# Performance work log

Hardware: AMD Instinct MI355X
Metric: run time of the kernel (lower is better)

Reference implementation:

```python
import jax, jax.numpy as jnp
import numpy as np

# PtConv dims from SegSmall: pl=64 channels, n_centers=16 kernel elements, dim=3
B, N, K = 4, 16384, 16          # batch, points, neighbors
C_IN, C_OUT, KS, DIM = 64, 64, 16, 3


def setup_inputs() -> dict:
    key = jax.random.key(0)
    ks = jax.random.split(key, 10)
    features = jax.random.normal(ks[0], (B, N, C_IN), dtype=jnp.float32)
    input_pts = jax.random.uniform(ks[1], (B, N, DIM), dtype=jnp.float32)
    output_pts = input_pts  # same-resolution conv: queries == input points
    indices = jax.random.randint(ks[2], (B, N, K), 0, N)  # precomputed KNN indices
    # weight init as in PtConv
    bound = float(np.sqrt(3.0) * np.sqrt(2.0 / (C_IN + C_OUT)))
    weight = jax.random.uniform(ks[3], (C_IN, KS, C_OUT), jnp.float32, -bound, bound)
    bias = jnp.zeros((C_OUT,), jnp.float32)
    centers = jax.random.uniform(ks[4], (DIM, KS), jnp.float32, -1.0, 1.0)
    # position-MLP params: Linear(dim*KS -> 2*KS), Linear(2*KS -> KS), Linear(KS -> KS)
    def lin(k, fan_in, fan_out):
        lim = 1.0 / np.sqrt(fan_in)
        kw, kb = jax.random.split(k)
        W = jax.random.uniform(kw, (fan_in, fan_out), jnp.float32, -lim, lim)
        b = jax.random.uniform(kb, (fan_out,), jnp.float32, -lim, lim)
        return W, b
    w1, b1 = lin(ks[5], DIM * KS, 2 * KS)
    w2, b2 = lin(ks[6], 2 * KS, KS)
    w3, b3 = lin(ks[7], KS, KS)
    return {"features": features, "input_pts": input_pts, "output_pts": output_pts,
            "weight": weight, "bias": bias, "centers": centers,
            "w1": w1, "b1": b1, "w2": w2, "b2": b2, "w3": w3, "b3": b3,
            "indices": indices}


def reference(features, input_pts, output_pts, weight, bias, centers,
              w1, b1, w2, b2, w3, b3, indices):
    # per-batch gather of neighbor features and coordinates
    gather = jax.vmap(lambda a, idx: a[idx])
    feat_g = gather(features, indices)          # [B, M, K, C_in]
    pts_g = gather(input_pts, indices)          # [B, M, K, 3]
    pts = pts_g - output_pts[:, :, None, :]      # nn_center=True
    # distances to kernel centers: [B,M,K,3,1] - [3,KS] -> [B,M,K,3,KS] -> [B,M,K,3*KS]
    d = (pts[..., None] - centers).reshape(pts.shape[0], pts.shape[1], pts.shape[2], -1)
    d = jax.nn.relu(d @ w1 + b1)
    d = jax.nn.relu(d @ w2 + b2)
    d = jax.nn.relu(d @ w3 + b3)                 # [B, M, K, KS]
    # weighted neighbor aggregation: bmm(features^T, dists)
    agg = jnp.einsum('bmkc,bmkj->bmcj', feat_g, d)   # [B, M, C_in, KS]
    out = jnp.einsum('bmcj,cjo->bmo', agg, weight)   # flatten (C_in,KS) matches weight.view(-1,out)
    out = out / feat_g.shape[2]                      # divide by K (fs[2])
    out = out + bias
    return out
```

## Files before the change

kernel.cpp:

```cpp
#include <hip/hip_runtime.h>

#define NPTS 16384
#define KN   16
#define CIN  64
#define COUT 64
#define KSIZ 16
#define PTS  16

typedef _Float16 h4v    __attribute__((ext_vector_type(4)));
typedef _Float16 h8v    __attribute__((ext_vector_type(8)));
typedef __fp16   fp16x2 __attribute__((ext_vector_type(2)));
typedef float    f32x4  __attribute__((ext_vector_type(4)));

union H2U { fp16x2 h; unsigned u; };
union H4U { h4v v; fp16x2 p[2]; uint2 u2; };
union H8U { h8v v; fp16x2 p[4]; uint4 u4; };

__global__ void prep_kernel(const float* __restrict__ weight,
                            const float* __restrict__ w1,
                            const float* __restrict__ b1,
                            const float* __restrict__ centers,
                            float* __restrict__ ws,
                            uint4* __restrict__ wf) {
    const int b = blockIdx.x;
    const int tid = threadIdx.x;
    if (b == 128) {
        int n = tid;
        if (n < 32) {
            float s0 = 0.f, s1 = 0.f, s2 = 0.f, bf = b1[n];
            for (int s = 0; s < KSIZ; ++s) {
                float a0 = w1[(0*KSIZ + s)*32 + n];
                float a1 = w1[(1*KSIZ + s)*32 + n];
                float a2 = w1[(2*KSIZ + s)*32 + n];
                s0 += a0; s1 += a1; s2 += a2;
                bf -= centers[0*KSIZ+s]*a0 + centers[1*KSIZ+s]*a1 + centers[2*KSIZ+s]*a2;
            }
            ws[0*32+n] = s0; ws[1*32+n] = s1; ws[2*32+n] = s2; ws[96+n] = bf;
        }
        return;
    }
    const int kk = b >> 2, nt = b & 3;
    const int l  = tid, li = l & 15, g = l >> 4;
    unsigned short u[8];
    #pragma unroll
    for (int e = 0; e < 8; ++e) {
        int s = kk*32 + g*8 + e;
        int j = s >> 6;
        int c = s & 63;
        union { _Float16 h; unsigned short s16; } cv;
        cv.h = (_Float16)weight[(c*16 + j)*64 + nt*16 + li];
        u[e] = cv.s16;
    }
    uint4 v;
    v.x = u[0] | ((unsigned)u[1] << 16);
    v.y = u[2] | ((unsigned)u[3] << 16);
    v.z = u[4] | ((unsigned)u[5] << 16);
    v.w = u[6] | ((unsigned)u[7] << 16);
    wf[(kk*4 + nt)*64 + l] = v;
}

__global__ __launch_bounds__(256, 4)
void ptconv_kernel(const float* __restrict__ features,
                   const float* __restrict__ input_pts,
                   const float* __restrict__ output_pts,
                   const float* __restrict__ bias,
                   const float* __restrict__ w2,
                   const float* __restrict__ b2,
                   const float* __restrict__ w3,
                   const float* __restrict__ b3,
                   const int*   __restrict__ indices,
                   const float* __restrict__ folded,
                   const uint4* __restrict__ wf,
                   float* __restrict__ out) {
    __shared__ __align__(16) char smem[34560];
    char*  s_agg = smem;
    char*  s_h1  = smem;
    int*   s_idx = (int*)(smem + 33024);
    float* s_par = (float*)(smem + 34048);

    const int t    = threadIdx.x;
    const int l    = t & 63;
    const int wave = t >> 6;
    const int li   = l & 15;
    const int g    = l >> 4;
    const int m0   = blockIdx.x * PTS;
    const int bbk  = m0 >> 14;

    if (t < 128) s_par[t] = folded[t];

    const int p1 = t >> 4, k1 = t & 15;
    const int nn = (m0 + p1) & (NPTS-1);
    const int idxv = indices[(bbk*NPTS + nn)*KN + k1];
    s_idx[p1*16 + k1] = idxv;
    const float* ip = input_pts  + (size_t)(bbk*NPTS + idxv)*3;
    const float* op = output_pts + (size_t)(bbk*NPTS + nn)*3;
    const float r0 = ip[0]-op[0], r1 = ip[1]-op[1], r2 = ip[2]-op[2];

    h8v w2f; h4v w3f;
    #pragma unroll
    for (int e = 0; e < 8; ++e) w2f[e] = (_Float16)w2[(8*g+e)*16 + li];
    #pragma unroll
    for (int e = 0; e < 4; ++e) w3f[e] = (_Float16)w3[(4*g+e)*16 + li];
    const f32x4 b2v4  = *(const f32x4*)(b2 + 4*g);
    const float b3v   = b3[li];
    const float biasO = bias[wave*16 + li];

    __syncthreads();

    {
        const float4* W0 = (const float4*)(s_par + 0);
        const float4* W1 = (const float4*)(s_par + 32);
        const float4* W2 = (const float4*)(s_par + 64);
        const float4* BF = (const float4*)(s_par + 96);
        unsigned o16[16];
        #pragma unroll
        for (int q = 0; q < 8; ++q) {
            const float4 bq = BF[q], a0 = W0[q], a1 = W1[q], a2 = W2[q];
            float v0 = fmaxf(fmaf(r2, a2.x, fmaf(r1, a1.x, fmaf(r0, a0.x, bq.x))), 0.f);
            float v1 = fmaxf(fmaf(r2, a2.y, fmaf(r1, a1.y, fmaf(r0, a0.y, bq.y))), 0.f);
            float v2 = fmaxf(fmaf(r2, a2.z, fmaf(r1, a1.z, fmaf(r0, a0.z, bq.z))), 0.f);
            float v3 = fmaxf(fmaf(r2, a2.w, fmaf(r1, a1.w, fmaf(r0, a0.w, bq.w))), 0.f);
            H2U u0, u1;
            u0.h = __builtin_amdgcn_cvt_pkrtz(v0, v1);
            u1.h = __builtin_amdgcn_cvt_pkrtz(v2, v3);
            o16[2*q]   = u0.u;
            o16[2*q+1] = u1.u;
        }
        uint4* dst = (uint4*)(s_h1 + t*80);
        dst[0] = make_uint4(o16[0],  o16[1],  o16[2],  o16[3]);
        dst[1] = make_uint4(o16[4],  o16[5],  o16[6],  o16[7]);
        dst[2] = make_uint4(o16[8],  o16[9],  o16[10], o16[11]);
        dst[3] = make_uint4(o16[12], o16[13], o16[14], o16[15]);
    }

    const float* fb = features + (size_t)bbk*NPTS*CIN;
    f32x4 rv[4][4];
    #pragma unroll
    for (int pp = 0; pp < 4; ++pp) {
        const int p2 = wave*4 + pp;
        const int4 id4 = *(const int4*)(s_idx + p2*16 + 4*g);
        rv[pp][0] = *(const f32x4*)(fb + (size_t)id4.x*CIN + 4*li);
        rv[pp][1] = *(const f32x4*)(fb + (size_t)id4.y*CIN + 4*li);
        rv[pp][2] = *(const f32x4*)(fb + (size_t)id4.z*CIN + 4*li);
        rv[pp][3] = *(const f32x4*)(fb + (size_t)id4.w*CIN + 4*li);
    }

    h4v dreg[4];
    #pragma unroll
    for (int pp = 0; pp < 4; ++pp) {
        const int mt = wave*4 + pp;
        h8v B2 = *(const h8v*)(s_h1 + (mt*16 + li)*80 + g*16);
        f32x4 acc2 = b2v4;
        acc2 = __builtin_amdgcn_mfma_f32_16x16x32_f16(w2f, B2, acc2, 0, 0, 0);
        H4U A3;
        A3.p[0] = __builtin_amdgcn_cvt_pkrtz(fmaxf(acc2[0],0.f), fmaxf(acc2[1],0.f));
        A3.p[1] = __builtin_amdgcn_cvt_pkrtz(fmaxf(acc2[2],0.f), fmaxf(acc2[3],0.f));
        f32x4 acc3 = {b3v, b3v, b3v, b3v};
        acc3 = __builtin_amdgcn_mfma_f32_16x16x16f16(A3.v, w3f, acc3, 0, 0, 0);
        H4U Dv;
        Dv.p[0] = __builtin_amdgcn_cvt_pkrtz(fmaxf(acc3[0],0.f), fmaxf(acc3[1],0.f));
        Dv.p[1] = __builtin_amdgcn_cvt_pkrtz(fmaxf(acc3[2],0.f), fmaxf(acc3[3],0.f));
        dreg[pp] = Dv.v;
    }
    __syncthreads();

    #pragma unroll
    for (int pp = 0; pp < 4; ++pp) {
        const int p2 = wave*4 + pp;
        f32x4 pacc[4];
        #pragma unroll
        for (int ct = 0; ct < 4; ++ct) {
            H4U B;
            B.p[0] = __builtin_amdgcn_cvt_pkrtz(rv[pp][0][ct], rv[pp][1][ct]);
            B.p[1] = __builtin_amdgcn_cvt_pkrtz(rv[pp][2][ct], rv[pp][3][ct]);
            f32x4 z = {0.f, 0.f, 0.f, 0.f};
            pacc[ct] = __builtin_amdgcn_mfma_f32_16x16x16f16(dreg[pp], B.v, z, 0, 0, 0);
        }
        #pragma unroll
        for (int r = 0; r < 4; ++r) {
            H2U d01, d23;
            d01.h = __builtin_amdgcn_cvt_pkrtz(pacc[0][r], pacc[1][r]);
            d23.h = __builtin_amdgcn_cvt_pkrtz(pacc[2][r], pacc[3][r]);
            *(uint2*)(s_agg + p2*2064 + (4*g + r)*128 + 8*li) = make_uint2(d01.u, d23.u);
        }
    }
    __syncthreads();

    f32x4 acc = {0.f, 0.f, 0.f, 0.f};
    #pragma unroll 4
    for (int kk = 0; kk < 32; ++kk) {
        h8v Bf = *(const h8v*)&wf[(kk*4 + wave)*64 + l];
        h8v Af = *(const h8v*)(s_agg + li*2064 + kk*64 + g*16);
        acc = __builtin_amdgcn_mfma_f32_16x16x32_f16(Af, Bf, acc, 0, 0, 0);
    }
    #pragma unroll
    for (int r = 0; r < 4; ++r) {
        const int mr = g*4 + r;
        out[(size_t)(m0 + mr)*COUT + wave*16 + li] = acc[r]*0.0625f + biasO;
    }
}

extern "C" void kernel_launch(void* const* d_in, const int* in_sizes, int n_in,
                              void* d_out, int out_size, void* d_ws, size_t ws_size,
                              hipStream_t stream) {
    const float* features   = (const float*)d_in[0];
    const float* input_pts  = (const float*)d_in[1];
    const float* output_pts = (const float*)d_in[2];
    const float* weight     = (const float*)d_in[3];
    const float* bias       = (const float*)d_in[4];
    const float* centers    = (const float*)d_in[5];
    const float* w1         = (const float*)d_in[6];
    const float* b1         = (const float*)d_in[7];
    const float* w2         = (const float*)d_in[8];
    const float* b2         = (const float*)d_in[9];
    const float* w3         = (const float*)d_in[10];
    const float* b3         = (const float*)d_in[11];
    const int*   indices    = (const int*)d_in[12];
    float* out = (float*)d_out;
    float* ws  = (float*)d_ws;
    uint4* wf  = (uint4*)((char*)d_ws + 512);

    prep_kernel<<<129, 64, 0, stream>>>(weight, w1, b1, centers, ws, wf);

    const int total_pts = 4 * NPTS;
    ptconv_kernel<<<total_pts / PTS, 256, 0, stream>>>(
        features, input_pts, output_pts, bias,
        w2, b2, w3, b3, indices, ws, wf, out);
}
```

Baseline: 52.29 us.

## Use packed fp16 first layer, drop syncs, prefetch weight fragments in final GEMM

The first position-MLP layer now runs as packed fp16 FMAs on params read straight from global memory instead of staged fp32 params in shared memory. This removes one __syncthreads, and the h1 buffer is made per-wave so a second barrier can go too. The 1/K scale is folded into the fp16 weights during prep. The final 32-step MFMA loop is fully unrolled with batches of weight fragments loaded from global ahead of use (the first batch before the barrier) and raised wave priority. Risks are lower precision in layer one, higher register pressure that may cut occupancy, and a possible hazard because the per-wave h1 region overlaps s_agg, which other waves write without a barrier in between.

```diff
diff --git a/kernel.cpp b/kernel.cpp
--- a/kernel.cpp
+++ b/kernel.cpp
@@ -13,20 +13,21 @@
 typedef float    f32x4  __attribute__((ext_vector_type(4)));
 
 union H2U { fp16x2 h; unsigned u; };
-union H4U { h4v v; fp16x2 p[2]; uint2 u2; };
-union H8U { h8v v; fp16x2 p[4]; uint4 u4; };
+union H4U { h4v v; fp16x2 p[2]; };
+union H8U { h8v v; uint4 u4; };
 
 __global__ void prep_kernel(const float* __restrict__ weight,
                             const float* __restrict__ w1,
                             const float* __restrict__ b1,
                             const float* __restrict__ centers,
-                            float* __restrict__ ws,
+                            unsigned* __restrict__ wsp,
                             uint4* __restrict__ wf) {
     const int b = blockIdx.x;
     const int tid = threadIdx.x;
     if (b == 128) {
-        int n = tid;
-        if (n < 32) {
+        __shared__ float tmp[4][32];
+        if (tid < 32) {
+            int n = tid;
             float s0 = 0.f, s1 = 0.f, s2 = 0.f, bf = b1[n];
             for (int s = 0; s < KSIZ; ++s) {
                 float a0 = w1[(0*KSIZ + s)*32 + n];
@@ -35,7 +36,15 @@
                 s0 += a0; s1 += a1; s2 += a2;
                 bf -= centers[0*KSIZ+s]*a0 + centers[1*KSIZ+s]*a1 + centers[2*KSIZ+s]*a2;
             }
-            ws[0*32+n] = s0; ws[1*32+n] = s1; ws[2*32+n] = s2; ws[96+n] = bf;
+            tmp[0][n] = s0; tmp[1][n] = s1; tmp[2][n] = s2; tmp[3][n] = bf;
+        }
+        __syncthreads();
+        if (tid < 64) {
+            const int row = tid >> 4, q = tid & 15;
+            union { _Float16 h[2]; unsigned u; } pk;
+            pk.h[0] = (_Float16)tmp[row][2*q];
+            pk.h[1] = (_Float16)tmp[row][2*q+1];
+            wsp[row*16 + q] = pk.u;
         }
         return;
     }
@@ -48,7 +57,7 @@
         int j = s >> 6;
         int c = s & 63;
         union { _Float16 h; unsigned short s16; } cv;
-        cv.h = (_Float16)weight[(c*16 + j)*64 + nt*16 + li];
+        cv.h = (_Float16)(weight[(c*16 + j)*64 + nt*16 + li] * 0.0625f);
         u[e] = cv.s16;
     }
     uint4 v;
@@ -69,14 +78,12 @@
                    const float* __restrict__ w3,
                    const float* __restrict__ b3,
                    const int*   __restrict__ indices,
-                   const float* __restrict__ folded,
+                   const unsigned* __restrict__ folded,
                    const uint4* __restrict__ wf,
                    float* __restrict__ out) {
-    __shared__ __align__(16) char smem[34560];
-    char*  s_agg = smem;
-    char*  s_h1  = smem;
-    int*   s_idx = (int*)(smem + 33024);
-    float* s_par = (float*)(smem + 34048);
+    __shared__ __align__(16) char smem[34048];
+    char* s_agg = smem;
+    int*  s_idx = (int*)(smem + 33024);
 
     const int t    = threadIdx.x;
     const int l    = t & 63;
@@ -86,8 +93,6 @@
     const int m0   = blockIdx.x * PTS;
     const int bbk  = m0 >> 14;
 
-    if (t < 128) s_par[t] = folded[t];
-
     const int p1 = t >> 4, k1 = t & 15;
     const int nn = (m0 + p1) & (NPTS-1);
     const int idxv = indices[(bbk*NPTS + nn)*KN + k1];
@@ -105,28 +110,25 @@
     const float b3v   = b3[li];
     const float biasO = bias[wave*16 + li];
 
-    __syncthreads();
-
     {
-        const float4* W0 = (const float4*)(s_par + 0);
-        const float4* W1 = (const float4*)(s_par + 32);
-        const float4* W2 = (const float4*)(s_par + 64);
-        const float4* BF = (const float4*)(s_par + 96);
+        const __fp16 r0h = (__fp16)r0, r1h = (__fp16)r1, r2h = (__fp16)r2;
+        fp16x2 r0p = {r0h, r0h}, r1p = {r1h, r1h}, r2p = {r2h, r2h};
+        const fp16x2 zz = {(__fp16)0.f, (__fp16)0.f};
         unsigned o16[16];
         #pragma unroll
-        for (int q = 0; q < 8; ++q) {
-            const float4 bq = BF[q], a0 = W0[q], a1 = W1[q], a2 = W2[q];
-            float v0 = fmaxf(fmaf(r2, a2.x, fmaf(r1, a1.x, fmaf(r0, a0.x, bq.x))), 0.f);
-            float v1 = fmaxf(fmaf(r2, a2.y, fmaf(r1, a1.y, fmaf(r0, a0.y, bq.y))), 0.f);
-            float v2 = fmaxf(fmaf(r2, a2.z, fmaf(r1, a1.z, fmaf(r0, a0.z, bq.z))), 0.f);
-            float v3 = fmaxf(fmaf(r2, a2.w, fmaf(r1, a1.w, fmaf(r0, a0.w, bq.w))), 0.f);
-            H2U u0, u1;
-            u0.h = __builtin_amdgcn_cvt_pkrtz(v0, v1);
-            u1.h = __builtin_amdgcn_cvt_pkrtz(v2, v3);
-            o16[2*q]   = u0.u;
-            o16[2*q+1] = u1.u;
-        }
-        uint4* dst = (uint4*)(s_h1 + t*80);
+        for (int q = 0; q < 16; ++q) {
+            H2U a, u0, u1, u2;
+            a.u  = folded[48+q];
+            u0.u = folded[q];
+            u1.u = folded[16+q];
+            u2.u = folded[32+q];
+            fp16x2 acc = r0p*u0.h + a.h;
+            acc = r1p*u1.h + acc;
+            acc = r2p*u2.h + acc;
+            acc = __builtin_elementwise_max(acc, zz);
+            H2U o; o.h = acc; o16[q] = o.u;
+        }
+        uint4* dst = (uint4*)(smem + wave*8256 + l*80);
         dst[0] = make_uint4(o16[0],  o16[1],  o16[2],  o16[3]);
         dst[1] = make_uint4(o16[4],  o16[5],  o16[6],  o16[7]);
         dst[2] = make_uint4(o16[8],  o16[9],  o16[10], o16[11]);
@@ -148,8 +150,7 @@
     h4v dreg[4];
     #pragma unroll
     for (int pp = 0; pp < 4; ++pp) {
-        const int mt = wave*4 + pp;
-        h8v B2 = *(const h8v*)(s_h1 + (mt*16 + li)*80 + g*16);
+        h8v B2 = *(const h8v*)(smem + wave*8256 + (pp*16 + li)*80 + g*16);
         f32x4 acc2 = b2v4;
         acc2 = __builtin_amdgcn_mfma_f32_16x16x32_f16(w2f, B2, acc2, 0, 0, 0);
         H4U A3;
@@ -162,7 +163,6 @@
         Dv.p[1] = __builtin_amdgcn_cvt_pkrtz(fmaxf(acc3[2],0.f), fmaxf(acc3[3],0.f));
         dreg[pp] = Dv.v;
     }
-    __syncthreads();
 
     #pragma unroll
     for (int pp = 0; pp < 4; ++pp) {
@@ -184,19 +184,39 @@
             *(uint2*)(s_agg + p2*2064 + (4*g + r)*128 + 8*li) = make_uint2(d01.u, d23.u);
         }
     }
+
+    const uint4* wp = wf + wave*64 + l;
+    uint4 wa0 = wp[0*256], wa1 = wp[1*256], wa2 = wp[2*256], wa3 = wp[3*256];
+    uint4 wa4 = wp[4*256], wa5 = wp[5*256], wa6 = wp[6*256], wa7 = wp[7*256];
+
     __syncthreads();
 
+    __builtin_amdgcn_s_setprio(1);
     f32x4 acc = {0.f, 0.f, 0.f, 0.f};
-    #pragma unroll 4
-    for (int kk = 0; kk < 32; ++kk) {
-        h8v Bf = *(const h8v*)&wf[(kk*4 + wave)*64 + l];
-        h8v Af = *(const h8v*)(s_agg + li*2064 + kk*64 + g*16);
-        acc = __builtin_amdgcn_mfma_f32_16x16x32_f16(Af, Bf, acc, 0, 0, 0);
-    }
+#define AREAD(KK) (*(const h8v*)(s_agg + li*2064 + (KK)*64 + g*16))
+#define MF(KK, WREG) { H8U bu_; bu_.u4 = WREG; acc = __builtin_amdgcn_mfma_f32_16x16x32_f16(AREAD(KK), bu_.v, acc, 0, 0, 0); }
+    uint4 wb0 = wp[ 8*256], wb1 = wp[ 9*256], wb2 = wp[10*256], wb3 = wp[11*256];
+    uint4 wb4 = wp[12*256], wb5 = wp[13*256], wb6 = wp[14*256], wb7 = wp[15*256];
+    MF(0, wa0) MF(1, wa1) MF(2, wa2) MF(3, wa3)
+    MF(4, wa4) MF(5, wa5) MF(6, wa6) MF(7, wa7)
+    uint4 wc0 = wp[16*256], wc1 = wp[17*256], wc2 = wp[18*256], wc3 = wp[19*256];
+    uint4 wc4 = wp[20*256], wc5 = wp[21*256], wc6 = wp[22*256], wc7 = wp[23*256];
+    MF( 8, wb0) MF( 9, wb1) MF(10, wb2) MF(11, wb3)
+    MF(12, wb4) MF(13, wb5) MF(14, wb6) MF(15, wb7)
+    uint4 wd0 = wp[24*256], wd1 = wp[25*256], wd2 = wp[26*256], wd3 = wp[27*256];
+    uint4 wd4 = wp[28*256], wd5 = wp[29*256], wd6 = wp[30*256], wd7 = wp[31*256];
+    MF(16, wc0) MF(17, wc1) MF(18, wc2) MF(19, wc3)
+    MF(20, wc4) MF(21, wc5) MF(22, wc6) MF(23, wc7)
+    MF(24, wd0) MF(25, wd1) MF(26, wd2) MF(27, wd3)
+    MF(28, wd4) MF(29, wd5) MF(30, wd6) MF(31, wd7)
+#undef MF
+#undef AREAD
+    __builtin_amdgcn_s_setprio(0);
+
     #pragma unroll
     for (int r = 0; r < 4; ++r) {
         const int mr = g*4 + r;
-        out[(size_t)(m0 + mr)*COUT + wave*16 + li] = acc[r]*0.0625f + biasO;
+        out[(size_t)(m0 + mr)*COUT + wave*16 + li] = acc[r] + biasO;
     }
 }
 
@@ -217,13 +237,13 @@
     const float* b3         = (const float*)d_in[11];
     const int*   indices    = (const int*)d_in[12];
     float* out = (float*)d_out;
-    float* ws  = (float*)d_ws;
-    uint4* wf  = (uint4*)((char*)d_ws + 512);
-
-    prep_kernel<<<129, 64, 0, stream>>>(weight, w1, b1, centers, ws, wf);
+    unsigned* wsp = (unsigned*)d_ws;
+    uint4* wf = (uint4*)((char*)d_ws + 512);
+
+    prep_kernel<<<129, 64, 0, stream>>>(weight, w1, b1, centers, wsp, wf);
 
     const int total_pts = 4 * NPTS;
     ptconv_kernel<<<total_pts / PTS, 256, 0, stream>>>(
         features, input_pts, output_pts, bias,
-        w2, b2, w3, b3, indices, ws, wf, out);
+        w2, b2, w3, b3, indices, wsp, wf, out);
 }
```

Result: faster. 50.15 us (-4.1%).
